# Kernel tuning notes

Hardware: AMD Instinct MI355X
Metric: run time of the kernel (lower is better)

## Reference

```python
import jax, jax.numpy as jnp
import numpy as np

B, S = 8, 2048
CHANNELS, DIM, HEADS = 256, 3, 6
TCH = CHANNELS * 2  # 512
EPS = 1e-5


def _linear_init(key, out_f, in_f):
    # torch nn.Linear default init: U(-1/sqrt(in_f), 1/sqrt(in_f)) for W and b
    k1, k2 = jax.random.split(key)
    bound = 1.0 / np.sqrt(in_f)
    w = jax.random.uniform(k1, (out_f, in_f), jnp.float32, -bound, bound)
    b = jax.random.uniform(k2, (out_f,), jnp.float32, -bound, bound)
    return w, b


def setup_inputs() -> dict:
    key = jax.random.key(0)
    ks = jax.random.split(key, 8)
    x = jax.random.normal(ks[0], (B, S, TCH), jnp.float32)
    wq, bq = _linear_init(ks[1], DIM, TCH)
    wk, bk = _linear_init(ks[2], DIM, TCH)
    wv, bv = _linear_init(ks[3], DIM, TCH)
    wo, bo = _linear_init(ks[4], TCH, HEADS * DIM)
    w1, b1 = _linear_init(ks[5], TCH, TCH)
    w2, b2 = _linear_init(ks[6], TCH, TCH)
    gamma = jnp.ones((TCH,), jnp.float32)
    beta = jnp.zeros((TCH,), jnp.float32)
    return {"x": x, "wq": wq, "bq": bq, "wk": wk, "bk": bk, "wv": wv, "bv": bv,
            "wo": wo, "bo": bo, "w1": w1, "b1": b1, "w2": w2, "b2": b2,
            "gamma": gamma, "beta": beta}


def _layernorm(x, gamma, beta):
    mu = jnp.mean(x, axis=-1, keepdims=True)
    var = jnp.mean(jnp.square(x - mu), axis=-1, keepdims=True)
    return (x - mu) * jax.lax.rsqrt(var + EPS) * gamma + beta


def reference(x, wq, bq, wk, bk, wv, bv, wo, bo, w1, b1, w2, b2, gamma, beta):
    # All heads share the same w_q/w_k/w_v, so one attention pass suffices;
    # concatenating HEADS copies reproduces the original math exactly.
    q = x @ wq.T + bq                      # [B,S,DIM]
    k = x @ wk.T + bk                      # [B,S,DIM]
    v = x @ wv.T + bv                      # [B,S,DIM]
    scores = jnp.einsum('bqd,bkd->bqk', q, k) / np.sqrt(DIM)  # [B,S,S]
    soft = jax.nn.softmax(scores, axis=-1)
    z = jnp.einsum('bqk,bkd->bqd', soft, v)  # [B,S,DIM]
    z = jnp.concatenate([z] * HEADS, axis=-1)  # [B,S,HEADS*DIM]
    z = z @ wo.T + bo                       # [B,S,TCH]
    r0 = x + (z @ w1.T + b1)
    r1 = _layernorm(r0, gamma, beta)
    r1 = r1 @ w2.T + b2
    r = r0 + r1
    return _layernorm(r, gamma, beta)
```

## Files before the change

### kernel.cpp

```cpp
#include <hip/hip_runtime.h>
#include <hip/hip_bf16.h>

#define TCH 512
#define MTOT 16384
#define SEQ 2048
#define LN_EPS 1e-5f

typedef __attribute__((ext_vector_type(8))) __bf16 bf16x8;
typedef __attribute__((ext_vector_type(4))) float f32x4;

__device__ __forceinline__ unsigned pkbf(float a, float b) {
  union { __hip_bfloat16 h; unsigned short u; } ca, cb;
  ca.h = __float2bfloat16(a); cb.h = __float2bfloat16(b);
  return (unsigned)ca.u | ((unsigned)cb.u << 16);
}
__device__ __forceinline__ float bf_lo(unsigned u) { return __uint_as_float(u << 16); }
__device__ __forceinline__ float bf_hi(unsigned u) { return __uint_as_float(u & 0xffff0000u); }

__device__ __forceinline__ bf16x8 cvt8(float4 a, float4 b) {
  union { __hip_bfloat16 h; __bf16 v; } u;
  bf16x8 r;
  u.h = __float2bfloat16(a.x); r[0] = u.v;
  u.h = __float2bfloat16(a.y); r[1] = u.v;
  u.h = __float2bfloat16(a.z); r[2] = u.v;
  u.h = __float2bfloat16(a.w); r[3] = u.v;
  u.h = __float2bfloat16(b.x); r[4] = u.v;
  u.h = __float2bfloat16(b.y); r[5] = u.v;
  u.h = __float2bfloat16(b.z); r[6] = u.v;
  u.h = __float2bfloat16(b.w); r[7] = u.v;
  return r;
}

#define QSCALE 0.8329517853860118f

__global__ __launch_bounds__(256) void prep_kernel(
    const float* __restrict__ w1, const float* __restrict__ w2,
    const float* __restrict__ wo, const float* __restrict__ bo,
    const float* __restrict__ wq, const float* __restrict__ bq,
    const float* __restrict__ wk, const float* __restrict__ bk,
    const float* __restrict__ wv, const float* __restrict__ bv,
    __hip_bfloat16* __restrict__ w1b, __hip_bfloat16* __restrict__ w2b,
    float4* __restrict__ wo_eff4,
    __hip_bfloat16* __restrict__ wqkvb, float* __restrict__ qkvbias)
{
  int i = blockIdx.x * 256 + threadIdx.x;
  w1b[i] = __float2bfloat16(w1[i]);
  w2b[i] = __float2bfloat16(w2[i]);
  if (i < TCH) {
    float s0 = 0.f, s1 = 0.f, s2 = 0.f;
    #pragma unroll
    for (int h = 0; h < 6; ++h) {
      s0 += wo[i*18 + h*3 + 0];
      s1 += wo[i*18 + h*3 + 1];
      s2 += wo[i*18 + h*3 + 2];
    }
    wo_eff4[i] = make_float4(s0, s1, s2, bo[i]);
  }
  if (i < 16 * TCH) {
    int row = i >> 9, k = i & 511;
    float v;
    if      (row < 3) v = wq[row * TCH + k] * QSCALE;
    else if (row < 6) v = wk[(row - 3) * TCH + k];
    else if (row < 9) v = wv[(row - 6) * TCH + k];
    else              v = 0.f;
    wqkvb[i] = __float2bfloat16(v);
  }
  if (i < 16) {
    float v;
    if      (i < 3) v = bq[i] * QSCALE;
    else if (i < 6) v = bk[i - 3];
    else if (i < 9) v = bv[i - 6];
    else            v = 0.f;
    qkvbias[i] = v;
  }
}

__global__ __launch_bounds__(256) void qkv_kernel(
    const float* __restrict__ x,
    const __hip_bfloat16* __restrict__ wqkvb, const float* __restrict__ qkvbias,
    float4* __restrict__ q4, uint4* __restrict__ kvp,
    __hip_bfloat16* __restrict__ xb)
{
  const int t = threadIdx.x, wv = t >> 6, ln = t & 63;
  const int l16 = ln & 15, quad = ln >> 4;
  const int row0 = blockIdx.x * 64 + wv * 16;

  bf16x8 bfr[16];
  #pragma unroll
  for (int ks = 0; ks < 16; ++ks)
    bfr[ks] = *reinterpret_cast<const bf16x8*>(wqkvb + l16 * TCH + ks * 32 + quad * 8);

  const float* xp = x + (size_t)(row0 + l16) * TCH + quad * 8;
  __hip_bfloat16* xo = xb + (size_t)(row0 + l16) * TCH + quad * 8;

  float4 xa0 = *(const float4*)xp,        xb0 = *(const float4*)(xp + 4);
  float4 xa1 = *(const float4*)(xp + 32), xb1 = *(const float4*)(xp + 36);
  f32x4 acc = {};
  #pragma unroll
  for (int ks = 0; ks < 16; ++ks) {
    float4 xa2 = {}, xb2 = {};
    if (ks < 14) {
      xa2 = *(const float4*)(xp + (ks + 2) * 32);
      xb2 = *(const float4*)(xp + (ks + 2) * 32 + 4);
    }
    bf16x8 af = cvt8(xa0, xb0);
    *reinterpret_cast<bf16x8*>(xo + ks * 32) = af;
    acc = __builtin_amdgcn_mfma_f32_16x16x32_bf16(af, bfr[ks], acc, 0, 0, 0);
    xa0 = xa1; xb0 = xb1; xa1 = xa2; xb1 = xb2;
  }

  __shared__ float tr[4][16][17];
  #pragma unroll
  for (int r = 0; r < 4; ++r) tr[wv][quad * 4 + r][l16] = acc[r];
  __syncthreads();

  if (ln < 32) {
    const int row  = ln & 15;
    const int grow = row0 + row;
    float c[9];
    #pragma unroll
    for (int j = 0; j < 9; ++j) c[j] = tr[wv][row][j] + qkvbias[j];
    if (ln < 16) {
      q4[grow] = make_float4(c[0], c[1], c[2], 0.f);
    } else {
      kvp[grow] = make_uint4(pkbf(c[3], c[4]), pkbf(c[5], c[6]), pkbf(c[7], c[8]), 0u);
    }
  }
}

__global__ __launch_bounds__(1024) void attn_kernel(
    const float4* __restrict__ q4, const uint4* __restrict__ kvp,
    const float4* __restrict__ wo_eff4,
    __hip_bfloat16* __restrict__ z2b)
{
  __shared__ float4 part[16 * 64];
  __shared__ float4 zbuf[64];
  __shared__ float4 woL[TCH];

  const int b    = blockIdx.x >> 5;
  const int qc   = blockIdx.x & 31;
  const int base = b * SEQ;
  const int tid  = threadIdx.x;
  for (int i = tid; i < TCH; i += 1024) woL[i] = wo_eff4[i];

  const int wave = tid >> 6;
  const int lane = tid & 63;
  const float4 q = q4[base + qc * 64 + lane];

  const int wu = __builtin_amdgcn_readfirstlane(wave);
  const uint4* kvw = kvp + base + wu * 128;

  float l[4] = {}, a0[4] = {}, a1[4] = {}, a2[4] = {};
  #pragma unroll 4
  for (int i = 0; i < 32; ++i) {
    #pragma unroll
    for (int s = 0; s < 4; ++s) {
      uint4 rec = kvw[s * 32 + i];
      float sc = bf_lo(rec.x) * q.x + bf_hi(rec.x) * q.y + bf_lo(rec.y) * q.z;
      float p = __builtin_amdgcn_exp2f(sc);
      l[s]  += p;
      a0[s] += p * bf_hi(rec.y);
      a1[s] += p * bf_lo(rec.z);
      a2[s] += p * bf_hi(rec.z);
    }
  }
  part[wave * 64 + lane] = make_float4(l[0]+l[1]+l[2]+l[3],
                                       a0[0]+a0[1]+a0[2]+a0[3],
                                       a1[0]+a1[1]+a1[2]+a1[3],
                                       a2[0]+a2[1]+a2[2]+a2[3]);
  __syncthreads();

  if (tid < 64) {
    float L = 0.f, A0 = 0.f, A1 = 0.f, A2 = 0.f;
    #pragma unroll
    for (int w = 0; w < 16; ++w) {
      float4 p = part[w * 64 + tid];
      L += p.x; A0 += p.y; A1 += p.z; A2 += p.w;
    }
    const float inv = 1.f / L;
    zbuf[tid] = make_float4(A0 * inv, A1 * inv, A2 * inv, 0.f);
  }
  __syncthreads();

  #pragma unroll
  for (int qi = 0; qi < 4; ++qi) {
    const int qloc = wave * 4 + qi;
    const float4 z = zbuf[qloc];
    unsigned* outr = (unsigned*)(z2b + (size_t)(base + qc * 64 + qloc) * TCH);
    #pragma unroll
    for (int it = 0; it < 4; ++it) {
      const int c = it * 128 + lane * 2;
      const float4 w0 = woL[c], w1 = woL[c + 1];
      outr[c >> 1] = pkbf(z.x*w0.x + z.y*w0.y + z.z*w0.z + w0.w,
                          z.x*w1.x + z.y*w1.y + z.z*w1.z + w1.w);
    }
  }
}

__global__ __launch_bounds__(256) void gemm_kernel(
    const __hip_bfloat16* __restrict__ A,
    const __hip_bfloat16* __restrict__ W,
    const float* __restrict__ bias,
    const __hip_bfloat16* __restrict__ res,
    __hip_bfloat16* __restrict__ Cout,
    float2* __restrict__ partial)
{
  __shared__ __align__(16) __hip_bfloat16 At[2][4][128][8];
  __shared__ __align__(16) __hip_bfloat16 Wt[2][4][128][8];
  __shared__ float redS[128][2];
  __shared__ float redQ[128][2];

  const int bx   = blockIdx.x;
  const int rb   = bx & 127, cb = bx >> 7;
  const int row0 = rb * 128, col0 = cb * 128;
  const int t    = threadIdx.x;
  const int w    = t >> 6, l = t & 63;
  const int l16  = l & 15, quad = l >> 4;
  const int wr   = w >> 1, wc = w & 1;
  const int srow = t & 127;
  const int sq0  = (t >> 7) << 1;

  auto stage = [&](int ks, int b) {
    #pragma unroll
    for (int j = 0; j < 2; ++j) {
      const int q = sq0 | j;
      __builtin_amdgcn_global_load_lds(
          (const __attribute__((address_space(1))) void*)(A + (size_t)(row0 + srow) * TCH + ks * 32 + q * 8),
          (__attribute__((address_space(3))) void*)&At[b][q][srow][0], 16, 0, 0);
      __builtin_amdgcn_global_load_lds(
          (const __attribute__((address_space(1))) void*)(W + (size_t)(col0 + srow) * TCH + ks * 32 + q * 8),
          (__attribute__((address_space(3))) void*)&Wt[b][q][srow][0], 16, 0, 0);
    }
  };

  f32x4 acc[4][4] = {};
  stage(0, 0);
  for (int ks = 0; ks < 16; ++ks) {
    const int cur = ks & 1;
    __syncthreads();
    if (ks < 15) stage(ks + 1, cur ^ 1);
    bf16x8 af[4], bf[4];
    #pragma unroll
    for (int mt = 0; mt < 4; ++mt)
      af[mt] = *reinterpret_cast<const bf16x8*>(&At[cur][quad][wr * 64 + mt * 16 + l16][0]);
    #pragma unroll
    for (int nt = 0; nt < 4; ++nt)
      bf[nt] = *reinterpret_cast<const bf16x8*>(&Wt[cur][quad][wc * 64 + nt * 16 + l16][0]);
    #pragma unroll
    for (int mt = 0; mt < 4; ++mt)
      #pragma unroll
      for (int nt = 0; nt < 4; ++nt)
        acc[mt][nt] = __builtin_amdgcn_mfma_f32_16x16x32_bf16(af[mt], bf[nt], acc[mt][nt], 0, 0, 0);
  }

  #pragma unroll
  for (int mt = 0; mt < 4; ++mt) {
    #pragma unroll
    for (int r = 0; r < 4; ++r) {
      const int lrow = wr * 64 + mt * 16 + quad * 4 + r;
      const int grow = row0 + lrow;
      float s = 0.f, sq = 0.f;
      #pragma unroll
      for (int nt = 0; nt < 4; ++nt) {
        const int col = col0 + wc * 64 + nt * 16 + l16;
        float v = acc[mt][nt][r] + bias[col] + __bfloat162float(res[(size_t)grow * TCH + col]);
        Cout[(size_t)grow * TCH + col] = __float2bfloat16(v);
        s += v; sq += v * v;
      }
      #pragma unroll
      for (int off = 1; off < 16; off <<= 1) {
        s  += __shfl_xor(s,  off, 64);
        sq += __shfl_xor(sq, off, 64);
      }
      if (l16 == 0) { redS[lrow][wc] = s; redQ[lrow][wc] = sq; }
    }
  }
  __syncthreads();

  if (t < 128) {
    partial[(size_t)cb * MTOT + row0 + t] =
        make_float2(redS[t][0] + redS[t][1], redQ[t][0] + redQ[t][1]);
  }
}

template<typename OUT_T>
__global__ __launch_bounds__(256) void ln_kernel(
    const __hip_bfloat16* __restrict__ Cin, const float2* __restrict__ partial,
    const float* __restrict__ gamma, const float* __restrict__ beta,
    OUT_T* __restrict__ out)
{
  const int t = threadIdx.x, wv = t >> 6, ln = t & 63;
  const int row = blockIdx.x * 4 + wv;

  float2 p0 = partial[row];
  float2 p1 = partial[MTOT + row];
  float2 p2 = partial[2 * MTOT + row];
  float2 p3 = partial[3 * MTOT + row];
  const float S = p0.x + p1.x + p2.x + p3.x;
  const float Q = p0.y + p1.y + p2.y + p3.y;
  const float mu  = S * (1.f / TCH);
  const float var = Q * (1.f / TCH) - mu * mu;
  const float rs  = rsqrtf(var + LN_EPS);

  const int c0 = ln * 8;
  bf16x8 vr = *reinterpret_cast<const bf16x8*>(Cin + (size_t)row * TCH + c0);
  float4 g0 = *(const float4*)(gamma + c0), g1 = *(const float4*)(gamma + c0 + 4);
  float4 b0 = *(const float4*)(beta  + c0), b1 = *(const float4*)(beta  + c0 + 4);

  float o[8];
  const float gg[8] = {g0.x,g0.y,g0.z,g0.w,g1.x,g1.y,g1.z,g1.w};
  const float bb[8] = {b0.x,b0.y,b0.z,b0.w,b1.x,b1.y,b1.z,b1.w};
  #pragma unroll
  for (int j = 0; j < 8; ++j) {
    union { __bf16 v; __hip_bfloat16 h; } u; u.v = vr[j];
    o[j] = (__bfloat162float(u.h) - mu) * rs * gg[j] + bb[j];
  }

  if constexpr (sizeof(OUT_T) == 2) {
    unsigned ov[4];
    #pragma unroll
    for (int j = 0; j < 4; ++j) ov[j] = pkbf(o[2*j], o[2*j+1]);
    *(uint4*)((__hip_bfloat16*)out + (size_t)row * TCH + c0) =
        make_uint4(ov[0], ov[1], ov[2], ov[3]);
  } else {
    float* op = (float*)out + (size_t)row * TCH + c0;
    *(float4*)op       = make_float4(o[0], o[1], o[2], o[3]);
    *(float4*)(op + 4) = make_float4(o[4], o[5], o[6], o[7]);
  }
}

extern "C" void kernel_launch(void* const* d_in, const int* in_sizes, int n_in,
                              void* d_out, int out_size, void* d_ws, size_t ws_size,
                              hipStream_t stream) {
  (void)in_sizes; (void)n_in; (void)out_size; (void)ws_size;
  const float* x     = (const float*)d_in[0];
  const float* wq    = (const float*)d_in[1];
  const float* bq    = (const float*)d_in[2];
  const float* wk    = (const float*)d_in[3];
  const float* bk    = (const float*)d_in[4];
  const float* wv    = (const float*)d_in[5];
  const float* bv    = (const float*)d_in[6];
  const float* wo    = (const float*)d_in[7];
  const float* bo    = (const float*)d_in[8];
  const float* w1    = (const float*)d_in[9];
  const float* b1    = (const float*)d_in[10];
  const float* w2    = (const float*)d_in[11];
  const float* b2    = (const float*)d_in[12];
  const float* gamma = (const float*)d_in[13];
  const float* beta  = (const float*)d_in[14];
  float* out = (float*)d_out;

  char* ws = (char*)d_ws;
  size_t off = 0;
  float4* q4      = (float4*)(ws + off); off += (size_t)MTOT * 16;
  uint4*  kvp     = (uint4*)(ws + off);  off += (size_t)MTOT * 16;
  float4* wo_eff4 = (float4*)(ws + off); off += (size_t)TCH * 16;
  __hip_bfloat16* w1b   = (__hip_bfloat16*)(ws + off); off += (size_t)TCH * TCH * 2;
  __hip_bfloat16* w2b   = (__hip_bfloat16*)(ws + off); off += (size_t)TCH * TCH * 2;
  __hip_bfloat16* wqkvb = (__hip_bfloat16*)(ws + off); off += (size_t)16 * TCH * 2;
  float*          qkvbias = (float*)(ws + off);        off += 64;
  __hip_bfloat16* xbb = (__hip_bfloat16*)(ws + off); off += (size_t)MTOT * TCH * 2;
  __hip_bfloat16* z2b = (__hip_bfloat16*)(ws + off); off += (size_t)MTOT * TCH * 2;
  __hip_bfloat16* r0b = (__hip_bfloat16*)(ws + off); off += (size_t)MTOT * TCH * 2;
  __hip_bfloat16* r1b = (__hip_bfloat16*)(ws + off); off += (size_t)MTOT * TCH * 2;
  __hip_bfloat16* rrb = (__hip_bfloat16*)(ws + off); off += (size_t)MTOT * TCH * 2;
  float2* part1 = (float2*)(ws + off); off += (size_t)4 * MTOT * 8;
  float2* part2 = (float2*)(ws + off); off += (size_t)4 * MTOT * 8;

  prep_kernel<<<(TCH*TCH)/256, 256, 0, stream>>>(
      w1, w2, wo, bo, wq, bq, wk, bk, wv, bv, w1b, w2b, wo_eff4, wqkvb, qkvbias);
  qkv_kernel<<<MTOT/64, 256, 0, stream>>>(x, wqkvb, qkvbias, q4, kvp, xbb);
  attn_kernel<<<MTOT/64, 1024, 0, stream>>>(q4, kvp, wo_eff4, z2b);
  gemm_kernel<<<512, 256, 0, stream>>>(z2b, w1b, b1, xbb, r0b, part1);
  ln_kernel<__hip_bfloat16><<<MTOT/4, 256, 0, stream>>>(r0b, part1, gamma, beta, r1b);
  gemm_kernel<<<512, 256, 0, stream>>>(r1b, w2b, b2, r0b, rrb, part2);
  ln_kernel<float><<<MTOT/4, 256, 0, stream>>>(rrb, part2, gamma, beta, out);
}
```

Before: 220.7 us.

## Fold W1 into rank-3 attention projection and fuse layernorms into producers

Precomputes W1·Wo_eff (a 512x4 matrix) so the first 512x512 GEMM collapses into a rank-3 update inside the attention epilogue, which also computes r0 and the first layernorm directly. The second GEMM is retiled to cover full 512-column rows per block so the final layernorm runs in its epilogue, which removes both ln kernels, the partial buffers and the xb/z2b intermediates. The cost is a wider per-block GEMM tile with more shared memory and registers, and a different rounding path because the folded weights stay in fp32.

New measurement: 183.1 us. -17.0%, faster.

```diff
diff --git a/kernel.cpp b/kernel.cpp
--- a/kernel.cpp
+++ b/kernel.cpp
@@ -34,17 +34,16 @@
 #define QSCALE 0.8329517853860118f
 
 __global__ __launch_bounds__(256) void prep_kernel(
-    const float* __restrict__ w1, const float* __restrict__ w2,
+    const float* __restrict__ w2,
     const float* __restrict__ wo, const float* __restrict__ bo,
     const float* __restrict__ wq, const float* __restrict__ bq,
     const float* __restrict__ wk, const float* __restrict__ bk,
     const float* __restrict__ wv, const float* __restrict__ bv,
-    __hip_bfloat16* __restrict__ w1b, __hip_bfloat16* __restrict__ w2b,
+    __hip_bfloat16* __restrict__ w2b,
     float4* __restrict__ wo_eff4,
     __hip_bfloat16* __restrict__ wqkvb, float* __restrict__ qkvbias)
 {
   int i = blockIdx.x * 256 + threadIdx.x;
-  w1b[i] = __float2bfloat16(w1[i]);
   w2b[i] = __float2bfloat16(w2[i]);
   if (i < TCH) {
     float s0 = 0.f, s1 = 0.f, s2 = 0.f;
@@ -75,11 +74,34 @@
   }
 }
 
+__global__ __launch_bounds__(256) void prep2_kernel(
+    const float* __restrict__ w1, const float* __restrict__ b1,
+    const float4* __restrict__ wo_eff4, float4* __restrict__ weff4)
+{
+  const int t = threadIdx.x, w = t >> 6, l = t & 63;
+  const int i = blockIdx.x * 4 + w;
+  float sx = 0.f, sy = 0.f, sz = 0.f, sw = 0.f;
+  #pragma unroll
+  for (int j = 0; j < 8; ++j) {
+    const int k = j * 64 + l;
+    const float a = w1[(size_t)i * TCH + k];
+    const float4 e = wo_eff4[k];
+    sx += a * e.x; sy += a * e.y; sz += a * e.z; sw += a * e.w;
+  }
+  #pragma unroll
+  for (int off = 1; off < 64; off <<= 1) {
+    sx += __shfl_xor(sx, off, 64);
+    sy += __shfl_xor(sy, off, 64);
+    sz += __shfl_xor(sz, off, 64);
+    sw += __shfl_xor(sw, off, 64);
+  }
+  if (l == 0) weff4[i] = make_float4(sx, sy, sz, sw + b1[i]);
+}
+
 __global__ __launch_bounds__(256) void qkv_kernel(
     const float* __restrict__ x,
     const __hip_bfloat16* __restrict__ wqkvb, const float* __restrict__ qkvbias,
-    float4* __restrict__ q4, uint4* __restrict__ kvp,
-    __hip_bfloat16* __restrict__ xb)
+    float4* __restrict__ q4, uint4* __restrict__ kvp)
 {
   const int t = threadIdx.x, wv = t >> 6, ln = t & 63;
   const int l16 = ln & 15, quad = ln >> 4;
@@ -91,7 +113,6 @@
     bfr[ks] = *reinterpret_cast<const bf16x8*>(wqkvb + l16 * TCH + ks * 32 + quad * 8);
 
   const float* xp = x + (size_t)(row0 + l16) * TCH + quad * 8;
-  __hip_bfloat16* xo = xb + (size_t)(row0 + l16) * TCH + quad * 8;
 
   float4 xa0 = *(const float4*)xp,        xb0 = *(const float4*)(xp + 4);
   float4 xa1 = *(const float4*)(xp + 32), xb1 = *(const float4*)(xp + 36);
@@ -104,7 +125,6 @@
       xb2 = *(const float4*)(xp + (ks + 2) * 32 + 4);
     }
     bf16x8 af = cvt8(xa0, xb0);
-    *reinterpret_cast<bf16x8*>(xo + ks * 32) = af;
     acc = __builtin_amdgcn_mfma_f32_16x16x32_bf16(af, bfr[ks], acc, 0, 0, 0);
     xa0 = xa1; xb0 = xb1; xa1 = xa2; xb1 = xb2;
   }
@@ -130,19 +150,17 @@
 
 __global__ __launch_bounds__(1024) void attn_kernel(
     const float4* __restrict__ q4, const uint4* __restrict__ kvp,
-    const float4* __restrict__ wo_eff4,
-    __hip_bfloat16* __restrict__ z2b)
+    const float* __restrict__ x, const float4* __restrict__ weff4,
+    const float* __restrict__ gamma, const float* __restrict__ beta,
+    __hip_bfloat16* __restrict__ r0b, __hip_bfloat16* __restrict__ r1b)
 {
   __shared__ float4 part[16 * 64];
   __shared__ float4 zbuf[64];
-  __shared__ float4 woL[TCH];
 
   const int b    = blockIdx.x >> 5;
   const int qc   = blockIdx.x & 31;
   const int base = b * SEQ;
   const int tid  = threadIdx.x;
-  for (int i = tid; i < TCH; i += 1024) woL[i] = wo_eff4[i];
-
   const int wave = tid >> 6;
   const int lane = tid & 63;
   const float4 q = q4[base + qc * 64 + lane];
@@ -182,90 +200,119 @@
   }
   __syncthreads();
 
+  const int c0 = lane * 8;
+  float4 wv[8];
+  #pragma unroll
+  for (int j = 0; j < 8; ++j) wv[j] = weff4[c0 + j];
+  const float4 g0  = *(const float4*)(gamma + c0);
+  const float4 g1  = *(const float4*)(gamma + c0 + 4);
+  const float4 be0 = *(const float4*)(beta  + c0);
+  const float4 be1 = *(const float4*)(beta  + c0 + 4);
+  const float gg[8] = {g0.x,g0.y,g0.z,g0.w,g1.x,g1.y,g1.z,g1.w};
+  const float bb[8] = {be0.x,be0.y,be0.z,be0.w,be1.x,be1.y,be1.z,be1.w};
+
   #pragma unroll
   for (int qi = 0; qi < 4; ++qi) {
     const int qloc = wave * 4 + qi;
+    const int grow = base + qc * 64 + qloc;
     const float4 z = zbuf[qloc];
-    unsigned* outr = (unsigned*)(z2b + (size_t)(base + qc * 64 + qloc) * TCH);
-    #pragma unroll
-    for (int it = 0; it < 4; ++it) {
-      const int c = it * 128 + lane * 2;
-      const float4 w0 = woL[c], w1 = woL[c + 1];
-      outr[c >> 1] = pkbf(z.x*w0.x + z.y*w0.y + z.z*w0.z + w0.w,
-                          z.x*w1.x + z.y*w1.y + z.z*w1.z + w1.w);
-    }
-  }
-}
-
-__global__ __launch_bounds__(256) void gemm_kernel(
+    const float* xr = x + (size_t)grow * TCH + c0;
+    const float4 x0 = *(const float4*)xr;
+    const float4 x1 = *(const float4*)(xr + 4);
+    const float xv[8] = {x0.x,x0.y,x0.z,x0.w,x1.x,x1.y,x1.z,x1.w};
+    float r0v[8], s = 0.f, sq = 0.f;
+    #pragma unroll
+    for (int j = 0; j < 8; ++j) {
+      float v = xv[j] + z.x * wv[j].x + z.y * wv[j].y + z.z * wv[j].z + wv[j].w;
+      r0v[j] = v; s += v; sq += v * v;
+    }
+    #pragma unroll
+    for (int off = 1; off < 64; off <<= 1) {
+      s  += __shfl_xor(s,  off, 64);
+      sq += __shfl_xor(sq, off, 64);
+    }
+    const float mu = s * (1.f / TCH);
+    const float rs = rsqrtf(sq * (1.f / TCH) - mu * mu + LN_EPS);
+    *(bf16x8*)(r0b + (size_t)grow * TCH + c0) =
+        cvt8(make_float4(r0v[0], r0v[1], r0v[2], r0v[3]),
+             make_float4(r0v[4], r0v[5], r0v[6], r0v[7]));
+    float r1v[8];
+    #pragma unroll
+    for (int j = 0; j < 8; ++j) r1v[j] = (r0v[j] - mu) * rs * gg[j] + bb[j];
+    *(bf16x8*)(r1b + (size_t)grow * TCH + c0) =
+        cvt8(make_float4(r1v[0], r1v[1], r1v[2], r1v[3]),
+             make_float4(r1v[4], r1v[5], r1v[6], r1v[7]));
+  }
+}
+
+__global__ __launch_bounds__(512) void gemm2_kernel(
     const __hip_bfloat16* __restrict__ A,
     const __hip_bfloat16* __restrict__ W,
     const float* __restrict__ bias,
     const __hip_bfloat16* __restrict__ res,
-    __hip_bfloat16* __restrict__ Cout,
-    float2* __restrict__ partial)
-{
-  __shared__ __align__(16) __hip_bfloat16 At[2][4][128][8];
-  __shared__ __align__(16) __hip_bfloat16 Wt[2][4][128][8];
-  __shared__ float redS[128][2];
-  __shared__ float redQ[128][2];
-
-  const int bx   = blockIdx.x;
-  const int rb   = bx & 127, cb = bx >> 7;
-  const int row0 = rb * 128, col0 = cb * 128;
+    const float* __restrict__ gamma, const float* __restrict__ beta,
+    float* __restrict__ out)
+{
+  __shared__ __align__(16) __hip_bfloat16 At[2][4][64][8];
+  __shared__ __align__(16) __hip_bfloat16 Wt[2][4][512][8];
+  __shared__ float redS[64][4], redQ[64][4];
+  __shared__ float muL[64], rsL[64];
+
+  const int row0 = blockIdx.x * 64;
   const int t    = threadIdx.x;
-  const int w    = t >> 6, l = t & 63;
+  const int w    = t >> 6;
+  const int l    = t & 63;
   const int l16  = l & 15, quad = l >> 4;
-  const int wr   = w >> 1, wc = w & 1;
-  const int srow = t & 127;
-  const int sq0  = (t >> 7) << 1;
-
-  auto stage = [&](int ks, int b) {
-    #pragma unroll
-    for (int j = 0; j < 2; ++j) {
-      const int q = sq0 | j;
+  const int wr   = w >> 2, wc = w & 3;
+
+  auto stage = [&](int ks, int buf) {
+    if (t < 256) {
+      const int srow = t & 63, qa = t >> 6;
       __builtin_amdgcn_global_load_lds(
-          (const __attribute__((address_space(1))) void*)(A + (size_t)(row0 + srow) * TCH + ks * 32 + q * 8),
-          (__attribute__((address_space(3))) void*)&At[b][q][srow][0], 16, 0, 0);
+          (const __attribute__((address_space(1))) void*)(A + (size_t)(row0 + srow) * TCH + ks * 32 + qa * 8),
+          (__attribute__((address_space(3))) void*)&At[buf][qa][srow][0], 16, 0, 0);
+    }
+    #pragma unroll
+    for (int j = 0; j < 4; ++j) {
       __builtin_amdgcn_global_load_lds(
-          (const __attribute__((address_space(1))) void*)(W + (size_t)(col0 + srow) * TCH + ks * 32 + q * 8),
-          (__attribute__((address_space(3))) void*)&Wt[b][q][srow][0], 16, 0, 0);
+          (const __attribute__((address_space(1))) void*)(W + (size_t)t * TCH + ks * 32 + j * 8),
+          (__attribute__((address_space(3))) void*)&Wt[buf][j][t][0], 16, 0, 0);
     }
   };
 
-  f32x4 acc[4][4] = {};
+  f32x4 acc[2][8] = {};
   stage(0, 0);
   for (int ks = 0; ks < 16; ++ks) {
     const int cur = ks & 1;
     __syncthreads();
     if (ks < 15) stage(ks + 1, cur ^ 1);
-    bf16x8 af[4], bf[4];
-    #pragma unroll
-    for (int mt = 0; mt < 4; ++mt)
-      af[mt] = *reinterpret_cast<const bf16x8*>(&At[cur][quad][wr * 64 + mt * 16 + l16][0]);
-    #pragma unroll
-    for (int nt = 0; nt < 4; ++nt)
-      bf[nt] = *reinterpret_cast<const bf16x8*>(&Wt[cur][quad][wc * 64 + nt * 16 + l16][0]);
-    #pragma unroll
-    for (int mt = 0; mt < 4; ++mt)
+    bf16x8 af[2], bfv[8];
+    #pragma unroll
+    for (int m = 0; m < 2; ++m)
+      af[m] = *reinterpret_cast<const bf16x8*>(&At[cur][quad][wr * 32 + m * 16 + l16][0]);
+    #pragma unroll
+    for (int n = 0; n < 8; ++n)
+      bfv[n] = *reinterpret_cast<const bf16x8*>(&Wt[cur][quad][wc * 128 + n * 16 + l16][0]);
+    #pragma unroll
+    for (int m = 0; m < 2; ++m)
       #pragma unroll
-      for (int nt = 0; nt < 4; ++nt)
-        acc[mt][nt] = __builtin_amdgcn_mfma_f32_16x16x32_bf16(af[mt], bf[nt], acc[mt][nt], 0, 0, 0);
-  }
-
-  #pragma unroll
-  for (int mt = 0; mt < 4; ++mt) {
+      for (int n = 0; n < 8; ++n)
+        acc[m][n] = __builtin_amdgcn_mfma_f32_16x16x32_bf16(af[m], bfv[n], acc[m][n], 0, 0, 0);
+  }
+
+  #pragma unroll
+  for (int m = 0; m < 2; ++m) {
     #pragma unroll
     for (int r = 0; r < 4; ++r) {
-      const int lrow = wr * 64 + mt * 16 + quad * 4 + r;
+      const int lrow = wr * 32 + m * 16 + quad * 4 + r;
       const int grow = row0 + lrow;
       float s = 0.f, sq = 0.f;
       #pragma unroll
-      for (int nt = 0; nt < 4; ++nt) {
-        const int col = col0 + wc * 64 + nt * 16 + l16;
-        float v = acc[mt][nt][r] + bias[col] + __bfloat162float(res[(size_t)grow * TCH + col]);
-        Cout[(size_t)grow * TCH + col] = __float2bfloat16(v);
-        s += v; sq += v * v;
+      for (int n = 0; n < 8; ++n) {
+        const int col = wc * 128 + n * 16 + l16;
+        float v = acc[m][n][r] + bias[col] +
+                  __bfloat162float(res[(size_t)grow * TCH + col]);
+        acc[m][n][r] = v; s += v; sq += v * v;
       }
       #pragma unroll
       for (int off = 1; off < 16; off <<= 1) {
@@ -276,56 +323,28 @@
     }
   }
   __syncthreads();
-
-  if (t < 128) {
-    partial[(size_t)cb * MTOT + row0 + t] =
-        make_float2(redS[t][0] + redS[t][1], redQ[t][0] + redQ[t][1]);
-  }
-}
-
-template<typename OUT_T>
-__global__ __launch_bounds__(256) void ln_kernel(
-    const __hip_bfloat16* __restrict__ Cin, const float2* __restrict__ partial,
-    const float* __restrict__ gamma, const float* __restrict__ beta,
-    OUT_T* __restrict__ out)
-{
-  const int t = threadIdx.x, wv = t >> 6, ln = t & 63;
-  const int row = blockIdx.x * 4 + wv;
-
-  float2 p0 = partial[row];
-  float2 p1 = partial[MTOT + row];
-  float2 p2 = partial[2 * MTOT + row];
-  float2 p3 = partial[3 * MTOT + row];
-  const float S = p0.x + p1.x + p2.x + p3.x;
-  const float Q = p0.y + p1.y + p2.y + p3.y;
-  const float mu  = S * (1.f / TCH);
-  const float var = Q * (1.f / TCH) - mu * mu;
-  const float rs  = rsqrtf(var + LN_EPS);
-
-  const int c0 = ln * 8;
-  bf16x8 vr = *reinterpret_cast<const bf16x8*>(Cin + (size_t)row * TCH + c0);
-  float4 g0 = *(const float4*)(gamma + c0), g1 = *(const float4*)(gamma + c0 + 4);
-  float4 b0 = *(const float4*)(beta  + c0), b1 = *(const float4*)(beta  + c0 + 4);
-
-  float o[8];
-  const float gg[8] = {g0.x,g0.y,g0.z,g0.w,g1.x,g1.y,g1.z,g1.w};
-  const float bb[8] = {b0.x,b0.y,b0.z,b0.w,b1.x,b1.y,b1.z,b1.w};
-  #pragma unroll
-  for (int j = 0; j < 8; ++j) {
-    union { __bf16 v; __hip_bfloat16 h; } u; u.v = vr[j];
-    o[j] = (__bfloat162float(u.h) - mu) * rs * gg[j] + bb[j];
-  }
-
-  if constexpr (sizeof(OUT_T) == 2) {
-    unsigned ov[4];
-    #pragma unroll
-    for (int j = 0; j < 4; ++j) ov[j] = pkbf(o[2*j], o[2*j+1]);
-    *(uint4*)((__hip_bfloat16*)out + (size_t)row * TCH + c0) =
-        make_uint4(ov[0], ov[1], ov[2], ov[3]);
-  } else {
-    float* op = (float*)out + (size_t)row * TCH + c0;
-    *(float4*)op       = make_float4(o[0], o[1], o[2], o[3]);
-    *(float4*)(op + 4) = make_float4(o[4], o[5], o[6], o[7]);
+  if (t < 64) {
+    const float S = redS[t][0] + redS[t][1] + redS[t][2] + redS[t][3];
+    const float Q = redQ[t][0] + redQ[t][1] + redQ[t][2] + redQ[t][3];
+    const float mu = S * (1.f / TCH);
+    muL[t] = mu;
+    rsL[t] = rsqrtf(Q * (1.f / TCH) - mu * mu + LN_EPS);
+  }
+  __syncthreads();
+  #pragma unroll
+  for (int m = 0; m < 2; ++m) {
+    #pragma unroll
+    for (int r = 0; r < 4; ++r) {
+      const int lrow = wr * 32 + m * 16 + quad * 4 + r;
+      const int grow = row0 + lrow;
+      const float mu = muL[lrow], rs = rsL[lrow];
+      #pragma unroll
+      for (int n = 0; n < 8; ++n) {
+        const int col = wc * 128 + n * 16 + l16;
+        out[(size_t)grow * TCH + col] =
+            (acc[m][n][r] - mu) * rs * gamma[col] + beta[col];
+      }
+    }
   }
 }
 
@@ -355,24 +374,17 @@
   float4* q4      = (float4*)(ws + off); off += (size_t)MTOT * 16;
   uint4*  kvp     = (uint4*)(ws + off);  off += (size_t)MTOT * 16;
   float4* wo_eff4 = (float4*)(ws + off); off += (size_t)TCH * 16;
-  __hip_bfloat16* w1b   = (__hip_bfloat16*)(ws + off); off += (size_t)TCH * TCH * 2;
+  float4* weff4   = (float4*)(ws + off); off += (size_t)TCH * 16;
   __hip_bfloat16* w2b   = (__hip_bfloat16*)(ws + off); off += (size_t)TCH * TCH * 2;
   __hip_bfloat16* wqkvb = (__hip_bfloat16*)(ws + off); off += (size_t)16 * TCH * 2;
   float*          qkvbias = (float*)(ws + off);        off += 64;
-  __hip_bfloat16* xbb = (__hip_bfloat16*)(ws + off); off += (size_t)MTOT * TCH * 2;
-  __hip_bfloat16* z2b = (__hip_bfloat16*)(ws + off); off += (size_t)MTOT * TCH * 2;
   __hip_bfloat16* r0b = (__hip_bfloat16*)(ws + off); off += (size_t)MTOT * TCH * 2;
   __hip_bfloat16* r1b = (__hip_bfloat16*)(ws + off); off += (size_t)MTOT * TCH * 2;
-  __hip_bfloat16* rrb = (__hip_bfloat16*)(ws + off); off += (size_t)MTOT * TCH * 2;
-  float2* part1 = (float2*)(ws + off); off += (size_t)4 * MTOT * 8;
-  float2* part2 = (float2*)(ws + off); off += (size_t)4 * MTOT * 8;
 
   prep_kernel<<<(TCH*TCH)/256, 256, 0, stream>>>(
-      w1, w2, wo, bo, wq, bq, wk, bk, wv, bv, w1b, w2b, wo_eff4, wqkvb, qkvbias);
-  qkv_kernel<<<MTOT/64, 256, 0, stream>>>(x, wqkvb, qkvbias, q4, kvp, xbb);
-  attn_kernel<<<MTOT/64, 1024, 0, stream>>>(q4, kvp, wo_eff4, z2b);
-  gemm_kernel<<<512, 256, 0, stream>>>(z2b, w1b, b1, xbb, r0b, part1);
-  ln_kernel<__hip_bfloat16><<<MTOT/4, 256, 0, stream>>>(r0b, part1, gamma, beta, r1b);
-  gemm_kernel<<<512, 256, 0, stream>>>(r1b, w2b, b2, r0b, rrb, part2);
-  ln_kernel<float><<<MTOT/4, 256, 0, stream>>>(rrb, part2, gamma, beta, out);
-}
+      w2, wo, bo, wq, bq, wk, bk, wv, bv, w2b, wo_eff4, wqkvb, qkvbias);
+  prep2_kernel<<<TCH/4, 256, 0, stream>>>(w1, b1, wo_eff4, weff4);
+  qkv_kernel<<<MTOT/64, 256, 0, stream>>>(x, wqkvb, qkvbias, q4, kvp);
+  attn_kernel<<<MTOT/64, 1024, 0, stream>>>(q4, kvp, x, weff4, gamma, beta, r0b, r1b);
+  gemm2_kernel<<<MTOT/64, 512, 0, stream>>>(r1b, w2b, b2, r0b, gamma, beta, out);
+}
```
